# Kernel optimization log

Hardware: AMD Instinct MI355X
Metric: run time of the kernel (lower is better)

Reference implementation:

```python
import jax, jax.numpy as jnp
import numpy as np


def setup_inputs() -> dict:
    key = jax.random.key(0)
    ks = jax.random.split(key, 10)
    B, T = 1024, 8192
    # X features: [time, current I, temperature T, voltage U]
    t = jnp.cumsum(jax.random.uniform(ks[0], (B, T, 1), jnp.float32) + 0.5, axis=1)  # increasing time
    feats = jax.random.normal(ks[1], (B, T, 3), jnp.float32)
    X = jnp.concatenate([t, feats], axis=-1)  # [B, T, 4]
    # SC: [Q (capacity), eta_0, R, SOC_init_base]; keep Q away from 0
    SC = jax.random.uniform(ks[2], (B, 4), jnp.float32, minval=0.5, maxval=1.5)
    std = 0.1
    # SOC_init_net: Linear(4,1) -> Softplus -> Linear(1,1), normal(0,0.1) weights, zero bias
    W1i = jax.random.normal(ks[3], (1, 4), jnp.float32) * std
    b1i = jnp.zeros((1,), jnp.float32)
    W2i = jax.random.normal(ks[4], (1, 1), jnp.float32) * std
    b2i = jnp.zeros((1,), jnp.float32)
    # eta_net: Linear(2,1) -> Softplus -> Linear(1,1)
    W1e = jax.random.normal(ks[5], (1, 2), jnp.float32) * std
    b1e = jnp.zeros((1,), jnp.float32)
    W2e = jax.random.normal(ks[6], (1, 1), jnp.float32) * std
    b2e = jnp.zeros((1,), jnp.float32)
    return {"X": X, "SC": SC, "W1i": W1i, "b1i": b1i, "W2i": W2i, "b2i": b2i,
            "W1e": W1e, "b1e": b1e, "W2e": W2e, "b2e": b2e}


def reference(X, SC, W1i, b1i, W2i, b2i, W1e, b1e, W2e, b2e):
    # X: [B, T, 4] = (t, I, Temp, U); SC: [B, 4] = (Q, eta_0, R, soc_base)
    I = X[..., 1:2]      # [B, T, 1]
    Temp = X[..., 2:3]   # [B, T, 1]
    U = X[..., 3:4]      # [B, T, 1]
    R = SC[..., 2:3]     # [B, 1]
    # SOC_init_net on first-timestep features
    feat0 = jnp.concatenate([I[:, 0, :], Temp[:, 0, :], U[:, 0, :], R], axis=-1)  # [B, 4]
    h0 = jax.nn.softplus(feat0 @ W1i.T + b1i)
    soc_net = h0 @ W2i.T + b2i                     # [B, 1]
    SOC_init = SC[..., 3:4] * (1.0 + soc_net)      # [B, 1]
    # eta_net over all timesteps
    feat = jnp.concatenate([I, Temp], axis=-1)     # [B, T, 2]
    h = jax.nn.softplus(feat @ W1e.T + b1e)
    delta_eta = h @ W2e.T + b2e                    # [B, T, 1]
    # ODE RHS: dSOC/dt = eta_0 * (1 + delta_eta) * I / (3600 * Q)
    Q = SC[..., 0:1][:, None, :]                   # [B, 1, 1]
    eta0 = SC[..., 1:2][:, None, :]                # [B, 1, 1]
    f = eta0 * (1.0 + delta_eta) * I / (3600.0 * Q)  # [B, T, 1]
    # Euler integration: y_{k+1} = y_k + (t_{k+1} - t_k) * f(x_k, y_k); f independent of y -> cumsum
    ts = X[..., 0:1]                               # [B, T, 1]
    dt = ts[:, 1:] - ts[:, :-1]                    # [B, T-1, 1]
    incr = dt * f[:, :-1]                          # [B, T-1, 1]
    zero = jnp.zeros_like(SOC_init)[:, None, :]    # [B, 1, 1]
    SOC = SOC_init[:, None, :] + jnp.concatenate([zero, jnp.cumsum(incr, axis=1)], axis=1)
    return SOC                                     # [B, T, 1]
```

## Files before the change

### kernel.cpp

```cpp
#include <hip/hip_runtime.h>
#include <type_traits>


static __device__ __forceinline__ float bf2f(unsigned int u) {
    union { unsigned int i; float f; } v;
    v.i = u << 16;
    return v.f;
}
static __device__ __forceinline__ unsigned short f2bf(float f) {
    union { unsigned int i; float f; } v;
    v.f = f;
    unsigned int x = v.i;
    return (unsigned short)((x + 0x7fffu + ((x >> 16) & 1u)) >> 16);
}
static __device__ __forceinline__ float sp_fast(float x) {
    return __logf(1.f + __expf(x));
}

struct F4 { float ts, I, Te, U; };
static __device__ __forceinline__ F4 dec(ushort4 x) {
    return {bf2f(x.x), bf2f(x.y), bf2f(x.z), bf2f(x.w)};
}
static __device__ __forceinline__ F4 dec(float4 x) {
    return {x.x, x.y, x.z, x.w};
}

template <bool BF16>
static __device__ __forceinline__ float ld(const void* p, int i) {
    return BF16 ? bf2f(((const unsigned short*)p)[i]) : ((const float*)p)[i];
}

constexpr int BLOCK = 256;
constexpr int PF    = 8;

template <int NC>
static __device__ void scan_ring(
    const float* __restrict__ X, const float* __restrict__ SC,
    const float* __restrict__ W1i, const float* __restrict__ b1i,
    const float* __restrict__ W2i, const float* __restrict__ b2i,
    const float* __restrict__ W1e, const float* __restrict__ b1e,
    const float* __restrict__ W2e, const float* __restrict__ b2e,
    float* __restrict__ outv, float* s_wtot, float* s_init)
{
    constexpr int T = NC * 256;
    constexpr int SPAN = T / 4;

    const int b    = blockIdx.x;
    const int tid  = threadIdx.x;
    const int lane = tid & 63;
    const int wave = tid >> 6;
    const int ws   = wave * SPAN;

    const float Q    = SC[b * 4 + 0];
    const float eta0 = SC[b * 4 + 1];
    const float R    = SC[b * 4 + 2];
    const float S3   = SC[b * 4 + 3];
    const float w1e0 = W1e[0];
    const float w1e1 = W1e[1];
    const float vb1e = b1e[0];
    const float coef = eta0 / (3600.f * Q);
    const float c2   = coef * W2e[0];
    const float c1   = coef * (1.f + b2e[0]);

    const float4* Xrow = (const float4*)X + (size_t)b * T;

    float4 ring[PF];
    #pragma unroll
    for (int j = 0; j < PF; ++j) ring[j] = Xrow[ws + j * 64 + lane];

    float ts_c, f_c;
    if (wave > 0) {
        const float4 vp = Xrow[ws - 1];
        const float hp = sp_fast(fmaf(vp.y, w1e0, fmaf(vp.z, w1e1, vb1e)));
        f_c  = fmaf(c2, hp, c1) * vp.y;
        ts_c = vp.x;
    } else {
        const float4 v0 = Xrow[0];
        ts_c = v0.x;
        f_c  = 0.f;
        const float pre = fmaf(v0.y, W1i[0],
                          fmaf(v0.z, W1i[1],
                          fmaf(v0.w, W1i[2],
                          fmaf(R, W1i[3], b1i[0]))));
        const float h0 = sp_fast(pre);
        if (lane == 0)
            *s_init = S3 * (1.f + fmaf(h0, W2i[0], b2i[0]));
    }

    float vals[NC];
    float carry = 0.f;
    #pragma unroll
    for (int c = 0; c < NC; ++c) {
        const float4 v = ring[c & (PF - 1)];
        if (c + PF < NC)
            ring[c & (PF - 1)] = Xrow[ws + (c + PF) * 64 + lane];

        const float f = fmaf(c2, sp_fast(fmaf(v.y, w1e0, fmaf(v.z, w1e1, vb1e))), c1) * v.y;

        float pts = __shfl_up(v.x, 1, 64);
        float pf  = __shfl_up(f,   1, 64);
        if (lane == 0) { pts = ts_c; pf = f_c; }
        float g = (v.x - pts) * pf;

        #pragma unroll
        for (int d = 1; d < 64; d <<= 1) {
            const float u = __shfl_up(g, d, 64);
            if (lane >= d) g += u;
        }
        g += carry;
        vals[c] = g;

        carry = __shfl(g, 63, 64);
        ts_c  = __shfl(v.x, 63, 64);
        f_c   = __shfl(f, 63, 64);
    }
    if (lane == 0) s_wtot[wave] = carry;
    __syncthreads();

    float base = *s_init;
    #pragma unroll
    for (int w = 0; w < 3; ++w)
        if (w < wave) base += s_wtot[w];

    float* op = outv + (size_t)b * T + ws + lane;
    #pragma unroll
    for (int c = 0; c < NC; ++c) op[c * 64] = vals[c] + base;
}

__global__ __launch_bounds__(BLOCK, 4) void socnet_reg(
    const void* __restrict__ X, const void* __restrict__ SC,
    const void* __restrict__ W1i, const void* __restrict__ b1i,
    const void* __restrict__ W2i, const void* __restrict__ b2i,
    const void* __restrict__ W1e, const void* __restrict__ b1e,
    const void* __restrict__ W2e, const void* __restrict__ b2e,
    void* __restrict__ out)
{
    __shared__ float s_wtot[4];
    __shared__ float s_init;
    scan_ring<32>((const float*)X, (const float*)SC,
                  (const float*)W1i, (const float*)b1i,
                  (const float*)W2i, (const float*)b2i,
                  (const float*)W1e, (const float*)b1e,
                  (const float*)W2e, (const float*)b2e,
                  (float*)out, s_wtot, &s_init);
}

template <bool BF16>
static __device__ void scan_serial(
    const void* __restrict__ Xv, const void* __restrict__ SCv,
    const void* __restrict__ W1i, const void* __restrict__ b1i,
    const void* __restrict__ W2i, const void* __restrict__ b2i,
    const void* __restrict__ W1e, const void* __restrict__ b1e,
    const void* __restrict__ W2e, const void* __restrict__ b2e,
    void* __restrict__ outv, int T,
    float* s_wts, float* s_wf, float* s_wsum, float* s_carr)
{
    using XVec = typename std::conditional<BF16, ushort4, float4>::type;
    const int b = blockIdx.x, tid = threadIdx.x;
    const int lane = tid & 63, wave = tid >> 6;
    const int ntile = (T + BLOCK - 1) / BLOCK;

    const float Q    = ld<BF16>(SCv, b * 4 + 0);
    const float eta0 = ld<BF16>(SCv, b * 4 + 1);
    const float R    = ld<BF16>(SCv, b * 4 + 2);
    const float S3   = ld<BF16>(SCv, b * 4 + 3);
    const float w1e0 = ld<BF16>(W1e, 0);
    const float w1e1 = ld<BF16>(W1e, 1);
    const float vb1e = ld<BF16>(b1e, 0);
    const float coef = eta0 / (3600.f * Q);
    const float c2   = coef * ld<BF16>(W2e, 0);
    const float c1   = coef * (1.f + ld<BF16>(b2e, 0));

    const XVec* Xrow = (const XVec*)Xv + (size_t)b * T;

    for (int tile = 0; tile < ntile; ++tile) {
        const int t = tile * BLOCK + tid;
        const bool act = t < T;
        F4 v = {0.f, 0.f, 0.f, 0.f};
        if (act) v = dec(Xrow[t]);
        const float f = fmaf(c2, sp_fast(fmaf(v.I, w1e0, fmaf(v.Te, w1e1, vb1e))), c1) * v.I;

        float pts = __shfl_up(v.ts, 1, 64);
        float pf  = __shfl_up(f, 1, 64);

        __syncthreads();
        if (lane == 63) { s_wts[wave] = v.ts; s_wf[wave] = f; }
        if (tile == 0 && tid == 0) {
            const float pre = fmaf(v.I, ld<BF16>(W1i, 0),
                              fmaf(v.Te, ld<BF16>(W1i, 1),
                              fmaf(v.U, ld<BF16>(W1i, 2),
                              fmaf(R, ld<BF16>(W1i, 3), ld<BF16>(b1i, 0)))));
            s_carr[0] = S3 * (1.f + fmaf(sp_fast(pre), ld<BF16>(W2i, 0), ld<BF16>(b2i, 0)));
        }
        __syncthreads();
        if (lane == 0) {
            if (wave == 0) { if (tile > 0) { pts = s_carr[1]; pf = s_carr[2]; } }
            else { pts = s_wts[wave - 1]; pf = s_wf[wave - 1]; }
        }
        float g = (t == 0 || !act) ? 0.f : (v.ts - pts) * pf;
        #pragma unroll
        for (int d = 1; d < 64; d <<= 1) {
            const float u = __shfl_up(g, d, 64);
            if (lane >= d) g += u;
        }
        if (lane == 63) s_wsum[wave] = g;
        __syncthreads();
        float soc = s_carr[0];
        #pragma unroll
        for (int w = 0; w < 3; ++w) if (w < wave) soc += s_wsum[w];
        soc += g;
        if (act) {
            if (BF16) ((unsigned short*)outv)[(size_t)b * T + t] = f2bf(soc);
            else      ((float*)outv)[(size_t)b * T + t] = soc;
        }
        __syncthreads();
        if (tid == BLOCK - 1) { s_carr[0] = soc; s_carr[1] = v.ts; s_carr[2] = f; }
    }
}

__global__ __launch_bounds__(BLOCK) void socnet_serial_k(
    const void* __restrict__ X, const void* __restrict__ SC,
    const void* __restrict__ W1i, const void* __restrict__ b1i,
    const void* __restrict__ W2i, const void* __restrict__ b2i,
    const void* __restrict__ W1e, const void* __restrict__ b1e,
    const void* __restrict__ W2e, const void* __restrict__ b2e,
    void* __restrict__ out, int T)
{
    __shared__ float s_wts[4], s_wf[4], s_wsum[4], s_carr[3];
    const unsigned int* scw = (const unsigned int*)SC;
    const float l0 = bf2f(scw[0] & 0xFFFFu), l1 = bf2f(scw[1] & 0xFFFFu);
    const float l2 = bf2f(scw[2] & 0xFFFFu), l3 = bf2f(scw[3] & 0xFFFFu);
    const bool isbf =
        (l0 >= 0.45f && l0 <= 1.55f) && (l1 >= 0.45f && l1 <= 1.55f) &&
        (l2 >= 0.45f && l2 <= 1.55f) && (l3 >= 0.45f && l3 <= 1.55f);
    if (isbf) scan_serial<true >(X, SC, W1i, b1i, W2i, b2i, W1e, b1e, W2e, b2e,
                                 out, T, s_wts, s_wf, s_wsum, s_carr);
    else      scan_serial<false>(X, SC, W1i, b1i, W2i, b2i, W1e, b1e, W2e, b2e,
                                 out, T, s_wts, s_wf, s_wsum, s_carr);
}

extern "C" void kernel_launch(void* const* d_in, const int* in_sizes, int n_in,
                              void* d_out, int out_size, void* d_ws, size_t ws_size,
                              hipStream_t stream) {
    const int B = in_sizes[1] / 4;
    const int T = in_sizes[0] / (B * 4);

    if (T == 8192) {
        socnet_reg<<<dim3(B), dim3(BLOCK), 0, stream>>>(
            d_in[0], d_in[1], d_in[2], d_in[3], d_in[4], d_in[5],
            d_in[6], d_in[7], d_in[8], d_in[9], d_out);
    } else {
        socnet_serial_k<<<dim3(B), dim3(BLOCK), 0, stream>>>(
            d_in[0], d_in[1], d_in[2], d_in[3], d_in[4], d_in[5],
            d_in[6], d_in[7], d_in[8], d_in[9], d_out, T);
    }
}
```

Baseline: 216.9 us.

## Process four consecutive timesteps per lane with serial prefix before wave scan

Each lane now owns four consecutive timesteps per chunk. It computes their local prefix serially, then runs a single wave-level shuffle scan over the per-lane totals. This cuts the number of shuffle scans per element by four and allows the output to be written as float4 vectors. The trade-off is that input loads become per-lane strided float4 reads, which are less coalesced, and register pressure rises because of the 8-entry ring of float4s.

Measured after the change: 215.0 us. About the same (-0.9%).

```diff
diff --git a/kernel.cpp b/kernel.cpp
--- a/kernel.cpp
+++ b/kernel.cpp
@@ -31,10 +31,9 @@
 }
 
 constexpr int BLOCK = 256;
-constexpr int PF    = 8;
-
-template <int NC>
-static __device__ void scan_ring(
+
+template <int NCH>
+static __device__ void scan_k4(
     const float* __restrict__ X, const float* __restrict__ SC,
     const float* __restrict__ W1i, const float* __restrict__ b1i,
     const float* __restrict__ W2i, const float* __restrict__ b2i,
@@ -42,8 +41,8 @@
     const float* __restrict__ W2e, const float* __restrict__ b2e,
     float* __restrict__ outv, float* s_wtot, float* s_init)
 {
-    constexpr int T = NC * 256;
-    constexpr int SPAN = T / 4;
+    constexpr int SPAN = NCH * 256;
+    constexpr int T    = SPAN * 4;
 
     const int b    = blockIdx.x;
     const int tid  = threadIdx.x;
@@ -64,9 +63,12 @@
 
     const float4* Xrow = (const float4*)X + (size_t)b * T;
 
-    float4 ring[PF];
-    #pragma unroll
-    for (int j = 0; j < PF; ++j) ring[j] = Xrow[ws + j * 64 + lane];
+    float4 ring[8];
+    #pragma unroll
+    for (int c = 0; c < 2; ++c)
+        #pragma unroll
+        for (int j = 0; j < 4; ++j)
+            ring[c * 4 + j] = Xrow[ws + c * 256 + lane * 4 + j];
 
     float ts_c, f_c;
     if (wave > 0) {
@@ -87,32 +89,50 @@
             *s_init = S3 * (1.f + fmaf(h0, W2i[0], b2i[0]));
     }
 
-    float vals[NC];
+    float vals[NCH * 4];
     float carry = 0.f;
     #pragma unroll
-    for (int c = 0; c < NC; ++c) {
-        const float4 v = ring[c & (PF - 1)];
-        if (c + PF < NC)
-            ring[c & (PF - 1)] = Xrow[ws + (c + PF) * 64 + lane];
-
-        const float f = fmaf(c2, sp_fast(fmaf(v.y, w1e0, fmaf(v.z, w1e1, vb1e))), c1) * v.y;
-
-        float pts = __shfl_up(v.x, 1, 64);
-        float pf  = __shfl_up(f,   1, 64);
+    for (int c = 0; c < NCH; ++c) {
+        const int s = (c & 1) * 4;
+        const float4 v0 = ring[s + 0];
+        const float4 v1 = ring[s + 1];
+        const float4 v2 = ring[s + 2];
+        const float4 v3 = ring[s + 3];
+        if (c + 2 < NCH) {
+            #pragma unroll
+            for (int j = 0; j < 4; ++j)
+                ring[s + j] = Xrow[ws + (c + 2) * 256 + lane * 4 + j];
+        }
+
+        const float f0 = fmaf(c2, sp_fast(fmaf(v0.y, w1e0, fmaf(v0.z, w1e1, vb1e))), c1) * v0.y;
+        const float f1 = fmaf(c2, sp_fast(fmaf(v1.y, w1e0, fmaf(v1.z, w1e1, vb1e))), c1) * v1.y;
+        const float f2 = fmaf(c2, sp_fast(fmaf(v2.y, w1e0, fmaf(v2.z, w1e1, vb1e))), c1) * v2.y;
+        const float f3 = fmaf(c2, sp_fast(fmaf(v3.y, w1e0, fmaf(v3.z, w1e1, vb1e))), c1) * v3.y;
+
+        float pts = __shfl_up(v3.x, 1, 64);
+        float pf  = __shfl_up(f3,   1, 64);
         if (lane == 0) { pts = ts_c; pf = f_c; }
-        float g = (v.x - pts) * pf;
-
+
+        const float g0 = (v0.x - pts) * pf;
+        const float g1 = fmaf(v1.x - v0.x, f0, g0);
+        const float g2 = fmaf(v2.x - v1.x, f1, g1);
+        const float g3 = fmaf(v3.x - v2.x, f2, g2);
+
+        float S = g3;
         #pragma unroll
         for (int d = 1; d < 64; d <<= 1) {
-            const float u = __shfl_up(g, d, 64);
-            if (lane >= d) g += u;
-        }
-        g += carry;
-        vals[c] = g;
-
-        carry = __shfl(g, 63, 64);
-        ts_c  = __shfl(v.x, 63, 64);
-        f_c   = __shfl(f, 63, 64);
+            const float u = __shfl_up(S, d, 64);
+            if (lane >= d) S += u;
+        }
+        const float tb = carry + (S - g3);
+        vals[c * 4 + 0] = g0 + tb;
+        vals[c * 4 + 1] = g1 + tb;
+        vals[c * 4 + 2] = g2 + tb;
+        vals[c * 4 + 3] = g3 + tb;
+
+        carry += __shfl(S, 63, 64);
+        ts_c   = __shfl(v3.x, 63, 64);
+        f_c    = __shfl(f3, 63, 64);
     }
     if (lane == 0) s_wtot[wave] = carry;
     __syncthreads();
@@ -122,9 +142,16 @@
     for (int w = 0; w < 3; ++w)
         if (w < wave) base += s_wtot[w];
 
-    float* op = outv + (size_t)b * T + ws + lane;
-    #pragma unroll
-    for (int c = 0; c < NC; ++c) op[c * 64] = vals[c] + base;
+    float4* orow = (float4*)(outv + (size_t)b * T);
+    #pragma unroll
+    for (int c = 0; c < NCH; ++c) {
+        float4 o;
+        o.x = vals[c * 4 + 0] + base;
+        o.y = vals[c * 4 + 1] + base;
+        o.z = vals[c * 4 + 2] + base;
+        o.w = vals[c * 4 + 3] + base;
+        orow[wave * (SPAN / 4) + c * 64 + lane] = o;
+    }
 }
 
 __global__ __launch_bounds__(BLOCK, 4) void socnet_reg(
@@ -137,12 +164,12 @@
 {
     __shared__ float s_wtot[4];
     __shared__ float s_init;
-    scan_ring<32>((const float*)X, (const float*)SC,
-                  (const float*)W1i, (const float*)b1i,
-                  (const float*)W2i, (const float*)b2i,
-                  (const float*)W1e, (const float*)b1e,
-                  (const float*)W2e, (const float*)b2e,
-                  (float*)out, s_wtot, &s_init);
+    scan_k4<8>((const float*)X, (const float*)SC,
+               (const float*)W1i, (const float*)b1i,
+               (const float*)W2i, (const float*)b2i,
+               (const float*)W1e, (const float*)b1e,
+               (const float*)W2e, (const float*)b2e,
+               (float*)out, s_wtot, &s_init);
 }
 
 template <bool BF16>
```
